# Optimization experiments

Hardware: AMD Instinct MI355X
Metric: run time of the kernel (lower is better)

Reference implementation:

```python
import jax, jax.numpy as jnp
import numpy as np

H_OUT = 16   # RoIRotate(height=16)
MAX_W = 192  # static pad width; setup bounds aspect so int(aspect*H_OUT) <= 184 < MAX_W


def setup_inputs() -> dict:
    key = jax.random.key(0)
    k1, k2, k3, k4, k5 = jax.random.split(key, 5)
    B, C, H, W, N = 4, 32, 512, 512, 64
    image = jax.random.normal(k1, (B, C, H, W), dtype=jnp.float32)
    left = jax.random.uniform(k2, (B, N), minval=0.0, maxval=W - 80.0)
    top = jax.random.uniform(k3, (B, N), minval=0.0, maxval=H - 80.0)
    bh = jax.random.uniform(k4, (B, N), minval=12.0, maxval=64.0)
    aspect = jax.random.uniform(k5, (B, N), minval=1.0, maxval=11.5)
    bw = aspect * bh
    theta = jnp.zeros((B, N), dtype=jnp.float32)  # present in box format, unused by forward
    boxes = jnp.stack([left, top, left + bw, top + bh, theta], axis=-1)
    return {"image": image, "boxes": boxes}


def _bilinear(img, x, y):
    # img: [C,H,W]; x,y: [N,Ho,Wo] sample coordinates (pixel units)
    C, H, W = img.shape
    x0 = jnp.clip(jnp.floor(x).astype(jnp.int32), 0, W - 1)
    x1 = jnp.clip(jnp.floor(x).astype(jnp.int32) + 1, 0, W - 1)
    y0 = jnp.clip(jnp.floor(y).astype(jnp.int32), 0, H - 1)
    y1 = jnp.clip(jnp.floor(y).astype(jnp.int32) + 1, 0, H - 1)
    ia = img[:, y0, x0]  # [C,N,Ho,Wo]
    ib = img[:, y1, x0]
    ic = img[:, y0, x1]
    idd = img[:, y1, x1]
    x0f, x1f = x0.astype(x.dtype), x1.astype(x.dtype)
    y0f, y1f = y0.astype(y.dtype), y1.astype(y.dtype)
    wa = (x1f - x) * (y1f - y)
    wb = (x1f - x) * (y - y0f)
    wc = (x - x0f) * (y1f - y)
    wd = (x - x0f) * (y - y0f)
    return ia * wa + ib * wb + ic * wc + idd * wd  # [C,N,Ho,Wo]


def reference(image, boxes):
    # image: [B,C,H,W]; boxes: [B,N,5] = (left, top, right, bottom, theta)
    B, C, H, W = image.shape
    N = boxes.shape[1]
    left, top = boxes[..., 0], boxes[..., 1]
    bw = boxes[..., 2] - boxes[..., 0]
    bh = boxes[..., 3] - boxes[..., 1]
    # per-box output width = int(aspect * height) (positive -> trunc == floor)
    width = (bw / bh * H_OUT).astype(jnp.int32)            # [B,N]
    each_w = bw / (width - 1).astype(jnp.float32)          # [B,N]
    each_h = bh / jnp.float32(H_OUT - 1)                   # [B,N]
    xx = jnp.arange(MAX_W, dtype=jnp.float32)[None, None, :] * each_w[..., None] + left[..., None]  # [B,N,MAX_W]
    yy = jnp.arange(H_OUT, dtype=jnp.float32)[None, None, :] * each_h[..., None] + top[..., None]   # [B,N,H_OUT]
    X = jnp.broadcast_to(xx[:, :, None, :], (B, N, H_OUT, MAX_W))
    Y = jnp.broadcast_to(yy[:, :, :, None], (B, N, H_OUT, MAX_W))
    samp = jax.vmap(_bilinear)(image, X, Y)                # [B,C,N,H_OUT,MAX_W]
    result = jnp.transpose(samp, (0, 2, 1, 3, 4))          # [B,N,C,H_OUT,MAX_W]
    colmask = jnp.arange(MAX_W)[None, None, :] < width[..., None]  # [B,N,MAX_W]
    result = result * colmask[:, :, None, None, :].astype(result.dtype)
    mask = colmask.astype(jnp.uint8)                       # [B,N,MAX_W]
    return result, mask
```

## Files before the change

### kernel.cpp

```cpp
#include <hip/hip_runtime.h>

namespace {
constexpr int kB = 4, kC = 32, kH = 512, kW = 512, kN = 64;
constexpr int kHout = 16, kMaxW = 192;
constexpr long long kResultElems = (long long)kB * kN * kC * kHout * kMaxW;
}

extern "C" __global__ __launch_bounds__(kMaxW) void roi_rotate(
    const float* __restrict__ image,
    const float* __restrict__ boxes,
    float* __restrict__ result,
    float* __restrict__ mask)
{
    const int blk = blockIdx.x;
    const int i  = blk & (kHout - 1);
    const int bn = blk >> 4;
    const int b  = bn >> 6;

    const float* bx = boxes + bn * 5;
    const float left = bx[0];
    const float top  = bx[1];
    const float bw   = __fsub_rn(bx[2], bx[0]);
    const float bh   = __fsub_rn(bx[3], bx[1]);
    const int width  = (int)(__fmul_rn(__fdiv_rn(bw, bh), (float)kHout));
    const float each_w = __fdiv_rn(bw, (float)(width - 1));
    const float each_h = __fdiv_rn(bh, (float)(kHout - 1));

    const int j = threadIdx.x;
    const float x = __fadd_rn(__fmul_rn((float)j, each_w), left);
    const float y = __fadd_rn(__fmul_rn((float)i, each_h), top);

    const int xf = (int)floorf(x);
    const int yf = (int)floorf(y);
    const int x0 = min(max(xf,     0), kW - 1);
    const int x1 = min(max(xf + 1, 0), kW - 1);
    const int y0 = min(max(yf,     0), kH - 1);
    const int y1 = min(max(yf + 1, 0), kH - 1);

    const float wx1 = (float)x1 - x;
    const float wx0 = x - (float)x0;
    const float wy1 = (float)y1 - y;
    const float wy0 = y - (float)y0;
    const float wa = wx1 * wy1;
    const float wb = wx1 * wy0;
    const float wc = wx0 * wy1;
    const float wd = wx0 * wy0;

    const bool valid = (j < width);

    float* op = result + (size_t)bn * (kC * kHout * kMaxW) + (size_t)i * kMaxW + j;

    if (valid) {
        const float* ch = image + (size_t)b * ((size_t)kC * kH * kW);
        const size_t oa = (size_t)y0 * kW + x0;
        const size_t ob = (size_t)y1 * kW + x0;
        const size_t oc = (size_t)y0 * kW + x1;
        const size_t od = (size_t)y1 * kW + x1;
        #pragma unroll 8
        for (int c = 0; c < kC; ++c) {
            const float va = ch[oa];
            const float vb = ch[ob];
            const float vc = ch[oc];
            const float vd = ch[od];
            op[0] = va * wa + vb * wb + vc * wc + vd * wd;
            ch += (size_t)kH * kW;
            op += kHout * kMaxW;
        }
    } else {
        #pragma unroll 8
        for (int c = 0; c < kC; ++c) {
            op[0] = 0.0f;
            op += kHout * kMaxW;
        }
    }

    if (i == 0) {
        mask[bn * kMaxW + j] = valid ? 1.0f : 0.0f;
    }
}

extern "C" void kernel_launch(void* const* d_in, const int* in_sizes, int n_in,
                              void* d_out, int out_size, void* d_ws, size_t ws_size,
                              hipStream_t stream) {
    const float* image = (const float*)d_in[0];
    const float* boxes = (const float*)d_in[1];
    float* result = (float*)d_out;
    float* mask   = result + kResultElems;

    dim3 grid(kB * kN * kHout);
    dim3 block(kMaxW);
    hipLaunchKernelGGL(roi_rotate, grid, block, 0, stream,
                       image, boxes, result, mask);
}
```

Before: 250.8 us.

## Stage the two source image rows in LDS with float4 loads before interpolating

For each pair of channels, the block cooperatively loads the span of the two needed source rows (y0, y1) covering the box's x-range into shared memory using aligned float4 loads. Threads then read their four bilinear taps from LDS instead of issuing four scattered global loads each. This replaces redundant, partly uncoalesced gathers with vectorized coalesced loads, at the cost of two __syncthreads per channel pair and 16 KB of LDS per block, which may lower occupancy.

```diff
diff --git a/kernel.cpp b/kernel.cpp
--- a/kernel.cpp
+++ b/kernel.cpp
@@ -12,6 +12,8 @@
     float* __restrict__ result,
     float* __restrict__ mask)
 {
+    __shared__ float ls[2][2][kW];
+
     const int blk = blockIdx.x;
     const int i  = blk & (kHout - 1);
     const int bn = blk >> 4;
@@ -48,30 +50,48 @@
 
     const bool valid = (j < width);
 
+    const int xlo = (min(max((int)floorf(left), 0), kW - 1)) & ~3;
+    const int xhi = min((int)floorf(__fadd_rn(left, bw)) + 1, kW - 1);
+    const int S    = xhi - xlo + 1;
+    const int nvec = (S + 3) >> 2;
+
+    const bool do_stage = (j < nvec);
+    const size_t row_off0 = (size_t)y0 * kW + xlo;
+    const size_t row_off1 = (size_t)y1 * kW + xlo;
+    const int lx0 = x0 - xlo;
+    const int lx1 = x1 - xlo;
+
     float* op = result + (size_t)bn * (kC * kHout * kMaxW) + (size_t)i * kMaxW + j;
+    const float* chbase = image + (size_t)b * ((size_t)kC * kH * kW);
+    constexpr size_t kChStride = (size_t)kH * kW;
+    constexpr int kOpStride = kHout * kMaxW;
 
-    if (valid) {
-        const float* ch = image + (size_t)b * ((size_t)kC * kH * kW);
-        const size_t oa = (size_t)y0 * kW + x0;
-        const size_t ob = (size_t)y1 * kW + x0;
-        const size_t oc = (size_t)y0 * kW + x1;
-        const size_t od = (size_t)y1 * kW + x1;
-        #pragma unroll 8
-        for (int c = 0; c < kC; ++c) {
-            const float va = ch[oa];
-            const float vb = ch[ob];
-            const float vc = ch[oc];
-            const float vd = ch[od];
-            op[0] = va * wa + vb * wb + vc * wc + vd * wd;
-            ch += (size_t)kH * kW;
-            op += kHout * kMaxW;
+    for (int c = 0; c < kC; c += 2) {
+        const float* p0 = chbase + (size_t)c * kChStride;
+        const float* p1 = p0 + kChStride;
+        if (do_stage) {
+            const int o = 4 * j;
+            const float4 v00 = *(const float4*)(p0 + row_off0 + o);
+            const float4 v01 = *(const float4*)(p0 + row_off1 + o);
+            const float4 v10 = *(const float4*)(p1 + row_off0 + o);
+            const float4 v11 = *(const float4*)(p1 + row_off1 + o);
+            *(float4*)&ls[0][0][o] = v00;
+            *(float4*)&ls[0][1][o] = v01;
+            *(float4*)&ls[1][0][o] = v10;
+            *(float4*)&ls[1][1][o] = v11;
         }
-    } else {
-        #pragma unroll 8
-        for (int c = 0; c < kC; ++c) {
-            op[0] = 0.0f;
-            op += kHout * kMaxW;
+        __syncthreads();
+        float out0 = 0.0f, out1 = 0.0f;
+        if (valid) {
+            out0 = ls[0][0][lx0] * wa + ls[0][1][lx0] * wb
+                 + ls[0][0][lx1] * wc + ls[0][1][lx1] * wd;
+            out1 = ls[1][0][lx0] * wa + ls[1][1][lx0] * wb
+                 + ls[1][0][lx1] * wc + ls[1][1][lx1] * wd;
         }
+        op[0]         = out0;
+        op[kOpStride] = out1;
+        op += 2 * kOpStride;
+        __syncthreads();
     }
 
     if (i == 0) {
```

Result: faster. 224.4 us (-10.6%).

## Stage bilinear source rows in LDS per wave with vectorized float4 loads

Applied to the files above, without the earlier changes.

Each wave now handles a subset of channels. For each channel it loads the two needed image rows covering the box x-span into LDS with coalesced float4 loads, then every lane computes its three output columns from LDS. This replaces four scattered gathers per output with contiguous row loads and shared reuse across columns. It adds LDS traffic and relies on wave-local sync through an inline s_waitcnt instead of a barrier. Channel parallelism within a block also drops to 3 waves looping over channels.

```diff
diff --git a/kernel.cpp b/kernel.cpp
--- a/kernel.cpp
+++ b/kernel.cpp
@@ -4,18 +4,25 @@
 constexpr int kB = 4, kC = 32, kH = 512, kW = 512, kN = 64;
 constexpr int kHout = 16, kMaxW = 192;
 constexpr long long kResultElems = (long long)kB * kN * kC * kHout * kMaxW;
+constexpr int kWaves = 3;
 }
 
-extern "C" __global__ __launch_bounds__(kMaxW) void roi_rotate(
+extern "C" __global__ __launch_bounds__(kWaves * 64) void roi_rotate(
     const float* __restrict__ image,
     const float* __restrict__ boxes,
     float* __restrict__ result,
     float* __restrict__ mask)
 {
+    __shared__ float ls[kWaves][2][kW];
+
     const int blk = blockIdx.x;
     const int i  = blk & (kHout - 1);
     const int bn = blk >> 4;
     const int b  = bn >> 6;
+
+    const int tid  = threadIdx.x;
+    const int w    = tid >> 6;
+    const int lane = tid & 63;
 
     const float* bx = boxes + bn * 5;
     const float left = bx[0];
@@ -26,56 +33,80 @@
     const float each_w = __fdiv_rn(bw, (float)(width - 1));
     const float each_h = __fdiv_rn(bh, (float)(kHout - 1));
 
-    const int j = threadIdx.x;
-    const float x = __fadd_rn(__fmul_rn((float)j, each_w), left);
     const float y = __fadd_rn(__fmul_rn((float)i, each_h), top);
-
-    const int xf = (int)floorf(x);
     const int yf = (int)floorf(y);
-    const int x0 = min(max(xf,     0), kW - 1);
-    const int x1 = min(max(xf + 1, 0), kW - 1);
     const int y0 = min(max(yf,     0), kH - 1);
     const int y1 = min(max(yf + 1, 0), kH - 1);
-
-    const float wx1 = (float)x1 - x;
-    const float wx0 = x - (float)x0;
     const float wy1 = (float)y1 - y;
     const float wy0 = y - (float)y0;
-    const float wa = wx1 * wy1;
-    const float wb = wx1 * wy0;
-    const float wc = wx0 * wy1;
-    const float wd = wx0 * wy0;
 
-    const bool valid = (j < width);
+    const int xlo = (min(max((int)floorf(left), 0), kW - 1)) & ~3;
+    const int xhi = min((int)floorf(__fadd_rn(left, bw)) + 1, kW - 1);
+    const int S   = xhi - xlo + 1;
 
-    float* op = result + (size_t)bn * (kC * kHout * kMaxW) + (size_t)i * kMaxW + j;
-
-    if (valid) {
-        const float* ch = image + (size_t)b * ((size_t)kC * kH * kW);
-        const size_t oa = (size_t)y0 * kW + x0;
-        const size_t ob = (size_t)y1 * kW + x0;
-        const size_t oc = (size_t)y0 * kW + x1;
-        const size_t od = (size_t)y1 * kW + x1;
-        #pragma unroll 8
-        for (int c = 0; c < kC; ++c) {
-            const float va = ch[oa];
-            const float vb = ch[ob];
-            const float vc = ch[oc];
-            const float vd = ch[od];
-            op[0] = va * wa + vb * wb + vc * wc + vd * wd;
-            ch += (size_t)kH * kW;
-            op += kHout * kMaxW;
-        }
-    } else {
-        #pragma unroll 8
-        for (int c = 0; c < kC; ++c) {
-            op[0] = 0.0f;
-            op += kHout * kMaxW;
-        }
+    int   lx0q[3], lx1q[3];
+    float waq[3], wbq[3], wcq[3], wdq[3];
+    bool  vq[3];
+    #pragma unroll
+    for (int q = 0; q < 3; ++q) {
+        const int j = 64 * q + lane;
+        const float x = __fadd_rn(__fmul_rn((float)j, each_w), left);
+        const int xf = (int)floorf(x);
+        const int x0 = min(max(xf,     0), kW - 1);
+        const int x1 = min(max(xf + 1, 0), kW - 1);
+        const float wx1 = (float)x1 - x;
+        const float wx0 = x - (float)x0;
+        lx0q[q] = x0 - xlo;
+        lx1q[q] = x1 - xlo;
+        waq[q] = wx1 * wy1;
+        wbq[q] = wx1 * wy0;
+        wcq[q] = wx0 * wy1;
+        wdq[q] = wx0 * wy0;
+        vq[q]  = (j < width);
     }
 
-    if (i == 0) {
-        mask[bn * kMaxW + j] = valid ? 1.0f : 0.0f;
+    const bool need0 = (4 * lane        < S);
+    const bool need1 = (4 * (lane + 64) < S);
+    const int  o0 = 4 * lane;
+    const int  o1 = 4 * (lane + 64);
+    const size_t r0 = (size_t)y0 * kW + xlo;
+    const size_t r1 = (size_t)y1 * kW + xlo;
+
+    const float* chbase = image + (size_t)b * ((size_t)kC * kH * kW);
+    constexpr size_t kChStride = (size_t)kH * kW;
+    float* opb = result + (size_t)bn * (kC * kHout * kMaxW) + (size_t)i * kMaxW;
+
+    for (int c = w; c < kC; c += kWaves) {
+        const float* p = chbase + (size_t)c * kChStride;
+        float4 a0, b0, a1, b1;
+        if (need0) { a0 = *(const float4*)(p + r0 + o0);
+                     b0 = *(const float4*)(p + r1 + o0); }
+        if (need1) { a1 = *(const float4*)(p + r0 + o1);
+                     b1 = *(const float4*)(p + r1 + o1); }
+        if (need0) { *(float4*)&ls[w][0][o0] = a0;
+                     *(float4*)&ls[w][1][o0] = b0; }
+        if (need1) { *(float4*)&ls[w][0][o1] = a1;
+                     *(float4*)&ls[w][1][o1] = b1; }
+        __asm__ volatile("s_waitcnt lgkmcnt(0)" ::: "memory");
+
+        float* op = opb + (size_t)c * (kHout * kMaxW);
+        #pragma unroll
+        for (int q = 0; q < 3; ++q) {
+            float out = 0.0f;
+            if (vq[q]) {
+                out = ls[w][0][lx0q[q]] * waq[q] + ls[w][1][lx0q[q]] * wbq[q]
+                    + ls[w][0][lx1q[q]] * wcq[q] + ls[w][1][lx1q[q]] * wdq[q];
+            }
+            op[64 * q + lane] = out;
+        }
+        __asm__ volatile("" ::: "memory");
+    }
+
+    if (i == 0 && w == 0) {
+        #pragma unroll
+        for (int q = 0; q < 3; ++q) {
+            mask[bn * kMaxW + 64 * q + lane] = vq[q] ? 1.0f : 0.0f;
+        }
     }
 }
 
@@ -88,7 +119,7 @@
     float* mask   = result + kResultElems;
 
     dim3 grid(kB * kN * kHout);
-    dim3 block(kMaxW);
+    dim3 block(kWaves * 64);
     hipLaunchKernelGGL(roi_rotate, grid, block, 0, stream,
                        image, boxes, result, mask);
 }
```

Measured after the change: 222.6 us. 1.13x faster.
